# Performance work log

Measured on AMD Instinct MI355X. Metric: run time of the kernel, lower is better.

The kernel has to match this reference:

```python
import jax, jax.numpy as jnp
import numpy as np

# Model constants (from init_kwargs / _select_heads)
H = 8          # heads for dim=1024
KR = 16        # read/write top-k
CHUNK = 128    # chunk size for chunked memory update
ETA = 0.1      # update rate
FORGET = 0.01  # decay_lambda -> forget_base per chunk
LWIN = 512     # local_window = K (use_bypass=True)


def _l2norm(t, eps=1e-6):
    return t / (jnp.linalg.norm(t, axis=-1, keepdims=True) + eps)


def setup_inputs() -> dict:
    key = jax.random.key(0)
    ks = jax.random.split(key, 5)
    B, T, D, K = 2, 2048, 1024, 512
    x = jax.random.normal(ks[0], (B, T, D), dtype=jnp.float32)
    W_qkv = jax.random.normal(ks[1], (3 * D, D), dtype=jnp.float32) / np.sqrt(D)
    b_qkv = jnp.zeros((3 * D,), dtype=jnp.float32)
    W_o = jax.random.normal(ks[2], (D, D), dtype=jnp.float32) / np.sqrt(D)
    b_o = jnp.zeros((D,), dtype=jnp.float32)
    S_init = jax.random.normal(ks[3], (K, D), dtype=jnp.float32) / np.sqrt(D)
    read_temperature = jnp.ones((1,), dtype=jnp.float32)
    return {"x": x, "W_qkv": W_qkv, "b_qkv": b_qkv, "W_o": W_o,
            "b_o": b_o, "S_init": S_init, "read_temperature": read_temperature}


def reference(x, W_qkv, b_qkv, W_o, b_o, S_init, read_temperature):
    B, T, D = x.shape
    K = S_init.shape[0]
    dh = D // H
    scale = 1.0 / np.sqrt(dh)
    temp = read_temperature[0]

    # fused qkv projection, split to heads [B,H,T,dh]
    qkv = x @ W_qkv.T + b_qkv
    q, k, v = jnp.split(qkv, 3, axis=-1)
    to_h = lambda t: t.reshape(B, T, H, dh).transpose(0, 2, 1, 3)
    qh, kh, vh = to_h(q), to_h(k), to_h(v)

    # initial slot state from S_init: [K, D] -> [H, K, dh] -> [B,H,K,dh]
    slot = S_init.reshape(K, H, dh).transpose(1, 0, 2)
    slot_k0 = jnp.broadcast_to(_l2norm(slot), (B, H, K, dh))
    slot_v0 = jnp.broadcast_to(slot, (B, H, K, dh))

    nc = T // CHUNK
    # [nc, B, H, C, dh]
    to_c = lambda t: t.reshape(B, H, nc, CHUNK, dh).transpose(2, 0, 1, 3, 4)
    qc, kc, vc = to_c(qh), to_c(kh), to_c(vh)

    bi_g = jnp.arange(B)[:, None, None, None]   # gather indices
    hi_g = jnp.arange(H)[None, :, None, None]
    bi_s = jnp.arange(B)[:, None, None]         # scatter indices
    hi_s = jnp.arange(H)[None, :, None]

    def chunk_step(carry, inp):
        slot_k, slot_v = carry
        qt, kt, vt = inp  # [B,H,C,dh]
        # ---- top-k sparse read from slot memory ----
        rscores = jnp.einsum('bhcd,bhkd->bhck', qt, slot_k) * scale / temp
        rv, ri = jax.lax.top_k(rscores, KR)
        rp = jax.nn.softmax(rv, axis=-1)                 # [B,H,C,KR]
        sel_v = slot_v[bi_g, hi_g, ri]                   # [B,H,C,KR,dh]
        read = jnp.einsum('bhck,bhckd->bhcd', rp, sel_v)
        # ---- top-k write with orthogonal update + decay ----
        k_hat = _l2norm(kt)
        wscores = jnp.einsum('bhcd,bhkd->bhck', k_hat, slot_k)
        wv, wi = jax.lax.top_k(wscores, KR)
        wp = jax.nn.softmax(wv, axis=-1)
        sel_k = slot_k[bi_g, hi_g, wi]                   # [B,H,C,KR,dh]
        proj = jnp.einsum('bhcd,bhckd->bhck', vt, sel_k)
        v_orth = vt[:, :, :, None, :] - proj[..., None] * sel_k
        dv = ETA * wp[..., None] * v_orth                # [B,H,C,KR,dh]
        dk = ETA * wp[..., None] * (k_hat[:, :, :, None, :] - sel_k)
        idx = wi.reshape(B, H, CHUNK * KR)
        slot_v = (1.0 - FORGET) * slot_v
        slot_v = slot_v.at[bi_s, hi_s, idx].add(dv.reshape(B, H, CHUNK * KR, dh))
        slot_k = _l2norm(slot_k.at[bi_s, hi_s, idx].add(dk.reshape(B, H, CHUNK * KR, dh)))
        return (slot_k, slot_v), read

    _, reads = jax.lax.scan(chunk_step, (slot_k0, slot_v0), (qc, kc, vc))
    reads = reads.transpose(1, 2, 0, 3, 4).reshape(B, H, T, dh)

    # ---- local bypass: block-causal sliding-window attention (window=LWIN) ----
    nb = T // LWIN
    qb = qh.reshape(B, H, nb, LWIN, dh)
    kb = kh.reshape(B, H, nb, LWIN, dh)
    vb = vh.reshape(B, H, nb, LWIN, dh)
    zpad = jnp.zeros_like(kb[:, :, :1])
    kcat = jnp.concatenate([jnp.concatenate([zpad, kb[:, :, :-1]], axis=2), kb], axis=3)
    vcat = jnp.concatenate([jnp.concatenate([zpad, vb[:, :, :-1]], axis=2), vb], axis=3)
    s = jnp.einsum('bhnqd,bhnkd->bhnqk', qb, kcat) * scale  # [B,H,nb,LWIN,2*LWIN]
    i = jnp.arange(LWIN)[:, None]
    j = jnp.arange(2 * LWIN)[None, :]
    base = (j <= LWIN + i) & (j > i)                        # causal + window
    blk = (jnp.arange(nb) > 0)[:, None, None] | (j >= LWIN)[None]
    mask = base[None] & blk                                 # [nb,LWIN,2*LWIN]
    s = jnp.where(mask[None, None], s, -1e30)
    a = jax.nn.softmax(s, axis=-1)
    local = jnp.einsum('bhnqk,bhnkd->bhnqd', a, vcat).reshape(B, H, T, dh)

    y = (reads + local).transpose(0, 2, 1, 3).reshape(B, T, D)
    return y @ W_o.T + b_o
```

## Files before the change

### kernel.cpp

```cpp
#include <hip/hip_runtime.h>

typedef unsigned short u16;
typedef unsigned int u32;
typedef unsigned long long u64;
typedef __attribute__((ext_vector_type(8))) short bf16x8;
typedef __attribute__((ext_vector_type(4))) float f32x4;

#define B2 2
#define T2 2048
#define D2 1024
#define H2 8
#define DH 128
#define KSL 512
#define CH 128
#define NCH 16
#define NBH 16
#define MAGIC 0x13579BDFu

__device__ __forceinline__ float bf2f(u32 h) { union { u32 u; float f; } x; x.u = h << 16; return x.f; }
__device__ __forceinline__ u16 f2bf(float f) {
  union { float f; u32 u; } x; x.f = f;
  return (u16)((x.u + 0x7FFFu + ((x.u >> 16) & 1u)) >> 16);
}
__device__ __forceinline__ u32 pack2(float a, float b) { return (u32)f2bf(a) | ((u32)f2bf(b) << 16); }

__device__ __forceinline__ u32 cload32(const void* p) {
  return __hip_atomic_load((u32*)p, __ATOMIC_RELAXED, __HIP_MEMORY_SCOPE_AGENT);
}
__device__ __forceinline__ void cstore32(void* p, u32 v) {
  __hip_atomic_store((u32*)p, v, __ATOMIC_RELAXED, __HIP_MEMORY_SCOPE_AGENT);
}
__device__ __forceinline__ u64 cload64(const void* p) {
  return __hip_atomic_load((u64*)p, __ATOMIC_RELAXED, __HIP_MEMORY_SCOPE_AGENT);
}
__device__ __forceinline__ void cstore64(void* p, u64 v) {
  __hip_atomic_store((u64*)p, v, __ATOMIC_RELAXED, __HIP_MEMORY_SCOPE_AGENT);
}
__device__ __forceinline__ float2 cloadf2(const float* p) {
  union { u64 q; float2 f; } x; x.q = cload64(p); return x.f;
}
__device__ __forceinline__ void cstoref2(float* p, float2 v) {
  union { float2 f; u64 q; } x; x.f = v; cstore64(p, x.q);
}

__global__ __launch_bounds__(256) void qkv_gemm(
    const float* __restrict__ x, const float* __restrict__ w,
    const float* __restrict__ bias, u16* __restrict__ qhb,
    u16* __restrict__ khb, u16* __restrict__ vhb) {
  __shared__ u16 As[128 * 72];
  __shared__ u16 Bs[128 * 72];
  const int tid = threadIdx.x;
  const int lane = tid & 63, wv = tid >> 6;
  const int quad = lane >> 4, l15 = lane & 15;
  const int m0 = blockIdx.y * 128, n0 = blockIdx.x * 128;
  const int wr = wv >> 1, wc = wv & 1;
  f32x4 acc[4][4];
#pragma unroll
  for (int i = 0; i < 4; ++i)
#pragma unroll
    for (int j = 0; j < 4; ++j) acc[i][j] = f32x4{0.f, 0.f, 0.f, 0.f};
  const int f4c = tid & 15, r0 = tid >> 4;
  for (int kt = 0; kt < 16; ++kt) {
#pragma unroll
    for (int i = 0; i < 8; ++i) {
      int row = r0 + i * 16;
      float4 a = *(const float4*)(x + (size_t)(m0 + row) * 1024 + kt * 64 + f4c * 4);
      float4 b = *(const float4*)(w + (size_t)(n0 + row) * 1024 + kt * 64 + f4c * 4);
      *(uint2*)(&As[row * 72 + f4c * 4]) = make_uint2(pack2(a.x, a.y), pack2(a.z, a.w));
      *(uint2*)(&Bs[row * 72 + f4c * 4]) = make_uint2(pack2(b.x, b.y), pack2(b.z, b.w));
    }
    __syncthreads();
#pragma unroll
    for (int ks = 0; ks < 2; ++ks) {
      bf16x8 af[4], bff[4];
#pragma unroll
      for (int rt = 0; rt < 4; ++rt)
        af[rt] = *(const bf16x8*)(&As[(wr * 64 + rt * 16 + l15) * 72 + ks * 32 + quad * 8]);
#pragma unroll
      for (int ct = 0; ct < 4; ++ct)
        bff[ct] = *(const bf16x8*)(&Bs[(wc * 64 + ct * 16 + l15) * 72 + ks * 32 + quad * 8]);
#pragma unroll
      for (int rt = 0; rt < 4; ++rt)
#pragma unroll
        for (int ct = 0; ct < 4; ++ct)
          acc[rt][ct] = __builtin_amdgcn_mfma_f32_16x16x32_bf16(af[rt], bff[ct], acc[rt][ct], 0, 0, 0);
    }
    __syncthreads();
  }
#pragma unroll
  for (int ct = 0; ct < 4; ++ct) {
    int n = n0 + wc * 64 + ct * 16 + l15;
    float bv = bias[n];
    int sec = n >> 10, rr2 = n & 1023, hh = rr2 >> 7, dd = rr2 & 127;
    u16* dst = (sec == 0) ? qhb : (sec == 1) ? khb : vhb;
#pragma unroll
    for (int rt = 0; rt < 4; ++rt)
#pragma unroll
      for (int rg = 0; rg < 4; ++rg) {
        int m = m0 + wr * 64 + rt * 16 + quad * 4 + rg;
        int bb = m >> 11, tt = m & 2047;
        dst[((size_t)(bb * 8 + hh) * T2 + tt) * DH + dd] = f2bf(acc[rt][ct][rg] + bv);
      }
  }
}

__global__ __launch_bounds__(256) void attn_kernel(
    const u16* __restrict__ qhb, const u16* __restrict__ khb,
    const u16* __restrict__ vhb, float* __restrict__ yin) {
  __shared__ u16 Pls[128 * 72];
  __shared__ u16 VT[128 * 72];
  const int tid = threadIdx.x;
  const int lane = tid & 63, wv = tid >> 6;
  const int quad = lane >> 4, l15 = lane & 15;
  const int bh = blockIdx.y, qt = blockIdx.x;
  const int t0 = qt * 128;
  const int b = bh >> 3, h = bh & 7;
  f32x4 Oa[2][8];
  float mrow[2][4], lrow[2][4];
#pragma unroll
  for (int rt = 0; rt < 2; ++rt) {
#pragma unroll
    for (int dt = 0; dt < 8; ++dt) Oa[rt][dt] = f32x4{0.f, 0.f, 0.f, 0.f};
#pragma unroll
    for (int rg = 0; rg < 4; ++rg) { mrow[rt][rg] = -1e30f; lrow[rt][rg] = 0.f; }
  }
  const u16* qbase = qhb + ((size_t)bh * T2 + t0) * DH;
  int j0 = t0 / 64 - 8; if (j0 < 0) j0 = 0;
  int j1 = t0 / 64 + 1;
  for (int jt = j0; jt <= j1; ++jt) {
    int kv0 = jt * 64;
    __syncthreads();
    {
      int r = tid & 63, dq = tid >> 6;
      const u16* vrow = vhb + ((size_t)bh * T2 + kv0 + r) * DH + dq * 32;
#pragma unroll
      for (int u = 0; u < 4; ++u) {
        uint4 pv = *(const uint4*)(vrow + u * 8);
        int d0 = dq * 32 + u * 8;
        VT[(d0 + 0) * 72 + r] = (u16)(pv.x); VT[(d0 + 1) * 72 + r] = (u16)(pv.x >> 16);
        VT[(d0 + 2) * 72 + r] = (u16)(pv.y); VT[(d0 + 3) * 72 + r] = (u16)(pv.y >> 16);
        VT[(d0 + 4) * 72 + r] = (u16)(pv.z); VT[(d0 + 5) * 72 + r] = (u16)(pv.z >> 16);
        VT[(d0 + 6) * 72 + r] = (u16)(pv.w); VT[(d0 + 7) * 72 + r] = (u16)(pv.w >> 16);
      }
    }
    f32x4 Sa[2][4];
#pragma unroll
    for (int rt = 0; rt < 2; ++rt)
#pragma unroll
      for (int ct = 0; ct < 4; ++ct) Sa[rt][ct] = f32x4{0.f, 0.f, 0.f, 0.f};
#pragma unroll
    for (int ks = 0; ks < 4; ++ks) {
      bf16x8 a0 = *(const bf16x8*)(qbase + (size_t)(wv * 32 + l15) * DH + ks * 32 + quad * 8);
      bf16x8 a1 = *(const bf16x8*)(qbase + (size_t)(wv * 32 + 16 + l15) * DH + ks * 32 + quad * 8);
#pragma unroll
      for (int ct = 0; ct < 4; ++ct) {
        bf16x8 bb = *(const bf16x8*)(khb + ((size_t)bh * T2 + kv0 + ct * 16 + l15) * DH + ks * 32 + quad * 8);
        Sa[0][ct] = __builtin_amdgcn_mfma_f32_16x16x32_bf16(a0, bb, Sa[0][ct], 0, 0, 0);
        Sa[1][ct] = __builtin_amdgcn_mfma_f32_16x16x32_bf16(a1, bb, Sa[1][ct], 0, 0, 0);
      }
    }
#pragma unroll
    for (int rt = 0; rt < 2; ++rt)
#pragma unroll
      for (int rg = 0; rg < 4; ++rg) {
        int row = wv * 32 + rt * 16 + quad * 4 + rg;
        int qp = t0 + row;
        float vals[4];
        float mx = -1e30f;
#pragma unroll
        for (int ct = 0; ct < 4; ++ct) {
          int kp = kv0 + ct * 16 + l15;
          float s = Sa[rt][ct][rg] * 0.08838834764831845f;
          bool ok = (kp <= qp) && (kp + 512 > qp);
          s = ok ? s : -1e30f;
          vals[ct] = s;
          mx = fmaxf(mx, s);
        }
#pragma unroll
        for (int sh = 1; sh < 16; sh <<= 1) mx = fmaxf(mx, __shfl_xor(mx, sh));
        float mold = mrow[rt][rg];
        float mnew = fmaxf(mold, mx);
        float alpha = __expf(mold - mnew);
        float rsum = 0.f;
        float pv_[4];
#pragma unroll
        for (int ct = 0; ct < 4; ++ct) {
          float p = (vals[ct] < -1e29f) ? 0.f : __expf(vals[ct] - mnew);
          pv_[ct] = p; rsum += p;
        }
#pragma unroll
        for (int sh = 1; sh < 16; sh <<= 1) rsum += __shfl_xor(rsum, sh);
        lrow[rt][rg] = lrow[rt][rg] * alpha + rsum;
        mrow[rt][rg] = mnew;
#pragma unroll
        for (int dt = 0; dt < 8; ++dt) Oa[rt][dt][rg] *= alpha;
#pragma unroll
        for (int ct = 0; ct < 4; ++ct) Pls[row * 72 + ct * 16 + l15] = f2bf(pv_[ct]);
      }
    __syncthreads();
#pragma unroll
    for (int ks = 0; ks < 2; ++ks) {
      bf16x8 a0 = *(const bf16x8*)(&Pls[(wv * 32 + l15) * 72 + ks * 32 + quad * 8]);
      bf16x8 a1 = *(const bf16x8*)(&Pls[(wv * 32 + 16 + l15) * 72 + ks * 32 + quad * 8]);
#pragma unroll
      for (int dt = 0; dt < 8; ++dt) {
        bf16x8 bb = *(const bf16x8*)(&VT[(dt * 16 + l15) * 72 + ks * 32 + quad * 8]);
        Oa[0][dt] = __builtin_amdgcn_mfma_f32_16x16x32_bf16(a0, bb, Oa[0][dt], 0, 0, 0);
        Oa[1][dt] = __builtin_amdgcn_mfma_f32_16x16x32_bf16(a1, bb, Oa[1][dt], 0, 0, 0);
      }
    }
  }
#pragma unroll
  for (int rt = 0; rt < 2; ++rt)
#pragma unroll
    for (int rg = 0; rg < 4; ++rg) {
      int row = wv * 32 + rt * 16 + quad * 4 + rg;
      float invl = 1.0f / lrow[rt][rg];
#pragma unroll
      for (int dt = 0; dt < 8; ++dt)
        yin[((size_t)b * T2 + t0 + row) * D2 + h * DH + dt * 16 + l15] = Oa[rt][dt][rg] * invl;
    }
}

struct ScanArgs {
  const u16* qhb; const u16* khb; const u16* vhb;
  float* yin; float* sk; float* sv; u16* skb; u16* khatb;
  u32* cnt; uint4* entries;
  u32* barcnt; u32* bargen; u32* ready;
  const float* sinit; const float* temp;
};

__device__ __forceinline__ void bh_barrier(u32* cnt, u32* gen) {
  asm volatile("" ::: "memory");
  __syncthreads();
  if (threadIdx.x == 0) {
    u32 g = cload32(gen);
    u32 a = __hip_atomic_fetch_add(cnt, 1u, __ATOMIC_RELAXED, __HIP_MEMORY_SCOPE_AGENT);
    if ((a & 15u) == 15u) {
      cstore32(gen, g + 1u);
    } else {
      while (cload32(gen) == g) __builtin_amdgcn_s_sleep(2);
    }
    __builtin_amdgcn_fence(__ATOMIC_ACQUIRE, "agent");
  }
  __syncthreads();
  asm volatile("" ::: "memory");
}

__device__ __forceinline__ void topk16(const float* rowp, int lane, volatile u64* candw,
                                       float& p_out, u32& idx_out) {
  u32 mono[8];
#pragma unroll
  for (int j = 0; j < 8; ++j) {
    float f = rowp[j * 64 + lane];
    u32 u = __float_as_uint(f);
    mono[j] = ((int)u < 0) ? ~u : (u | 0x80000000u);
  }
  u32 mx = mono[0];
#pragma unroll
  for (int j = 1; j < 8; ++j) mx = max(mx, mono[j]);
  u32 s = mx;
#pragma unroll
  for (int k = 2; k <= 64; k <<= 1) {
#pragma unroll
    for (int j = k >> 1; j > 0; j >>= 1) {
      u32 o = (u32)__shfl_xor((int)s, j);
      bool keep_min = (((lane & k) == 0) == ((lane & j) == 0));
      u32 mn = min(s, o), mxx = max(s, o);
      s = keep_min ? mn : mxx;
    }
  }
  u32 thr = (u32)__shfl((int)s, 48);
  u32 base = 0;
#pragma unroll
  for (int j = 0; j < 8; ++j) {
    bool pred = (mono[j] >= thr);
    u64 mask = __ballot(pred);
    u32 pos = base + (u32)__popcll(mask & ((1ull << lane) - 1ull));
    if (pred && pos < 64u)
      candw[pos] = (((u64)mono[j]) << 32) | (u64)(0xFFFFFFFFu - (u32)(j * 64 + lane));
    base += (u32)__popcll(mask);
  }
  __threadfence_block();
  u32 cntc = base < 64u ? base : 64u;
  u64 key = ((u32)lane < cntc) ? candw[lane] : 0ull;
#pragma unroll
  for (int k = 2; k <= 64; k <<= 1) {
#pragma unroll
    for (int j = k >> 1; j > 0; j >>= 1) {
      u64 o = __shfl_xor(key, j);
      bool keep_min = (((lane & k) == 0) == ((lane & j) == 0));
      u64 mn = key < o ? key : o;
      u64 mxx = key < o ? o : key;
      key = keep_min ? mn : mxx;
    }
  }
  u32 um = (u32)(key >> 32);
  float val = __uint_as_float((um & 0x80000000u) ? (um & 0x7FFFFFFFu) : ~um);
  idx_out = 0xFFFFFFFFu - (u32)(key & 0xFFFFFFFFull);
  float mtop = __shfl(val, 63);
  float e = __expf(val - mtop);
  float ssum = e;
#pragma unroll
  for (int sh = 1; sh < 16; sh <<= 1) ssum += __shfl_xor(ssum, sh);
  p_out = e / ssum;
}

__global__ __launch_bounds__(512, 2) void scan_kernel(ScanArgs A) {
  const int tid = threadIdx.x;
  const int lane = tid & 63, wv = tid >> 6;
  const int quad = lane >> 4, l15 = lane & 15;
  const int xcd = blockIdx.x & 7;
  const int wi = blockIdx.x >> 3;
  const int bh = xcd * 2 + (wi >> 4);
  const int blk = wi & 15;
  const int b = bh >> 3, h = bh & 7;
  __shared__ u16 khat_ls[8 * 136];
  __shared__ float scores_r[8 * 520];
  __shared__ float scores_w[8 * 520];
  __shared__ u64 cand[8][64];

  const float invtemp = 1.0f / A.temp[0];
  const float sc_r = 0.08838834764831845f * invtemp;

#pragma unroll 1
  for (int i = 0; i < 4; ++i) {
    int s = blk * 32 + wv * 4 + i;
    float2 v2 = *(const float2*)(A.sinit + (size_t)s * 1024 + h * 128 + lane * 2);
    float ssq = v2.x * v2.x + v2.y * v2.y;
#pragma unroll
    for (int sh = 1; sh < 64; sh <<= 1) ssq += __shfl_xor(ssq, sh);
    float inv = 1.0f / (sqrtf(ssq) + 1e-6f);
    size_t off = ((size_t)bh * KSL + s) * DH + lane * 2;
    cstoref2(A.sk + off, make_float2(v2.x * inv, v2.y * inv));
    cstoref2(A.sv + off, v2);
    cstore32(A.skb + off, pack2(v2.x * inv, v2.y * inv));
    if (lane == 0) cstore32(&A.cnt[bh * KSL + s], 0u);
  }
  if (blk == 0 && tid == 0) { cstore32(A.barcnt + bh, 0u); cstore32(A.bargen + bh, 0u); }
  __syncthreads();
  if (tid == 0) {
    cstore32(&A.ready[bh * 16 + blk], MAGIC);
    for (int i = 0; i < 16; ++i)
      while (cload32(&A.ready[bh * 16 + i]) != MAGIC) __builtin_amdgcn_s_sleep(2);
    __builtin_amdgcn_fence(__ATOMIC_ACQUIRE, "agent");
  }
  __syncthreads();

  u32* bcnt = A.barcnt + bh;
  u32* bgen = A.bargen + bh;

#pragma unroll 1
  for (int ci = 0; ci < NCH; ++ci) {
    const int t0base = ci * CH;
    const int c = blk * 8 + wv;
    const int trow = t0base + c;
    {
      u32 kraw = *(const u32*)(A.khb + ((size_t)bh * T2 + trow) * DH + lane * 2);
      float k0 = bf2f(kraw & 0xFFFFu), k1 = bf2f(kraw >> 16);
      float ssq = k0 * k0 + k1 * k1;
#pragma unroll
      for (int sh = 1; sh < 64; sh <<= 1) ssq += __shfl_xor(ssq, sh);
      float inv = 1.0f / (sqrtf(ssq) + 1e-6f);
      u32 pk = pack2(k0 * inv, k1 * inv);
      *(u32*)(&khat_ls[wv * 136 + lane * 2]) = pk;
      cstore32(A.khatb + ((size_t)bh * CH + c) * DH + lane * 2, pk);
    }
    __syncthreads();
    {
      const u16* qbase = A.qhb + ((size_t)bh * T2 + t0base + blk * 8) * DH;
      const u16* sbase = A.skb + (size_t)bh * KSL * DH;
      f32x4 acc[4];
#pragma unroll
      for (int ct = 0; ct < 4; ++ct) acc[ct] = f32x4{0.f, 0.f, 0.f, 0.f};
#pragma unroll
      for (int ks = 0; ks < 4; ++ks) {
        bf16x8 a;
        if (l15 < 8)
          a = *(const bf16x8*)(qbase + (size_t)l15 * DH + ks * 32 + quad * 8);
        else
          a = *(const bf16x8*)(&khat_ls[(l15 - 8) * 136 + ks * 32 + quad * 8]);
#pragma unroll
        for (int ct = 0; ct < 4; ++ct) {
          bf16x8 bb = *(const bf16x8*)(sbase + (size_t)(wv * 64 + ct * 16 + l15) * DH + ks * 32 + quad * 8);
          acc[ct] = __builtin_amdgcn_mfma_f32_16x16x32_bf16(a, bb, acc[ct], 0, 0, 0);
        }
      }
#pragma unroll
      for (int ct = 0; ct < 4; ++ct)
#pragma unroll
        for (int rg = 0; rg < 4; ++rg) {
          int m = quad * 4 + rg;
          int col = wv * 64 + ct * 16 + l15;
          if (m < 8) scores_r[m * 520 + col] = acc[ct][rg] * sc_r;
          else       scores_w[(m - 8) * 520 + col] = acc[ct][rg];
        }
    }
    __syncthreads();
    {
      float p; u32 sidx;
      topk16(&scores_r[wv * 520], lane, cand[wv], p, sidx);
      float acc0 = 0.f, acc1 = 0.f;
      const float* svb = A.sv + (size_t)bh * KSL * DH;
#pragma unroll
      for (int r = 0; r < 16; ++r) {
        float pr = __shfl(p, 63 - r);
        u32 ir = (u32)__shfl((int)sidx, 63 - r);
        float2 vv = *(const float2*)(svb + (size_t)ir * DH + lane * 2);
        acc0 += pr * vv.x; acc1 += pr * vv.y;
      }
      {
        float* yp = A.yin + ((size_t)b * T2 + trow) * D2 + h * DH + lane * 2;
        float2 y0 = cloadf2(yp);
        cstoref2(yp, make_float2(y0.x + acc0, y0.y + acc1));
      }

      float wp; u32 widx;
      topk16(&scores_w[wv * 520], lane, cand[wv], wp, widx);
      const int r = lane >> 2, g = lane & 3;
      float wr = __shfl(wp, 63 - r);
      u32 ir = (u32)__shfl((int)widx, 63 - r);
      const float* kb = A.sk + ((size_t)bh * KSL + ir) * DH + g * 32;
      const u16* vb = A.vhb + ((size_t)bh * T2 + trow) * DH + g * 32;
      float part = 0.f;
#pragma unroll
      for (int u2 = 0; u2 < 4; ++u2) {
        uint4 vvp = *(const uint4*)(vb + u2 * 8);
        float4 k0 = *(const float4*)(kb + u2 * 8);
        float4 k1 = *(const float4*)(kb + u2 * 8 + 4);
        part += bf2f(vvp.x & 0xFFFFu) * k0.x + bf2f(vvp.x >> 16) * k0.y
              + bf2f(vvp.y & 0xFFFFu) * k0.z + bf2f(vvp.y >> 16) * k0.w
              + bf2f(vvp.z & 0xFFFFu) * k1.x + bf2f(vvp.z >> 16) * k1.y
              + bf2f(vvp.w & 0xFFFFu) * k1.z + bf2f(vvp.w >> 16) * k1.w;
      }
      part += __shfl_xor(part, 1);
      part += __shfl_xor(part, 2);
      if (g == 0) {
        u32 pos = __hip_atomic_fetch_add(&A.cnt[bh * KSL + ir], 1u,
                                         __ATOMIC_RELAXED, __HIP_MEMORY_SCOPE_AGENT);
        if (pos < 128u) {
          u32* e = (u32*)(A.entries + ((size_t)bh * KSL + ir) * 128 + pos);
          cstore64(e, (u64)(u32)c | ((u64)__float_as_uint(wr) << 32));
          cstore32(e + 2, __float_as_uint(part));
        }
      }
    }
    bh_barrier(bcnt, bgen);
    {
      u32 n4[4]; size_t soff4[4];
      uint4 eL0[4], eL1[4];
#pragma unroll
      for (int i = 0; i < 4; ++i) {
        soff4[i] = (size_t)bh * KSL + blk * 32 + wv * 4 + i;
        n4[i] = cload32(&A.cnt[soff4[i]]);
        const uint4* eb = A.entries + soff4[i] * 128;
        eL0[i] = eb[lane];
        eL1[i] = eb[64 + lane];
      }
#pragma unroll
      for (int i = 0; i < 4; ++i) {
        size_t roff = soff4[i] * DH + lane * 2;
        float2 V = *(const float2*)(A.sv + roff);
        float2 Kr = *(const float2*)(A.sk + roff);
        u32 nd = n4[i] < 128u ? n4[i] : 128u;
        float dv0 = 0, dv1 = 0, dk0 = 0, dk1 = 0;
#pragma unroll 1
        for (u32 b2 = 0; b2 < nd; b2 += 16) {
          u32 m = nd - b2; if (m > 16u) m = 16u;
          u32 sx = (b2 < 64u) ? eL0[i].x : eL1[i].x;
          u32 sy = (b2 < 64u) ? eL0[i].y : eL1[i].y;
          u32 sz = (b2 < 64u) ? eL0[i].z : eL1[i].z;
          u32 vr[16], hr[16];
#pragma unroll
          for (int j = 0; j < 16; ++j) if (j < (int)m) {
            u32 src = (b2 + (u32)j) & 63u;
            u32 c2 = (u32)__shfl((int)sx, (int)src);
            vr[j] = *(const u32*)(A.vhb + ((size_t)bh * T2 + t0base + c2) * DH + lane * 2);
            hr[j] = *(const u32*)(A.khatb + ((size_t)bh * CH + c2) * DH + lane * 2);
          }
#pragma unroll
          for (int j = 0; j < 16; ++j) if (j < (int)m) {
            u32 src = (b2 + (u32)j) & 63u;
            float wpe = __uint_as_float((u32)__shfl((int)sy, (int)src));
            float pj = __uint_as_float((u32)__shfl((int)sz, (int)src));
            dv0 += wpe * (bf2f(vr[j] & 0xFFFFu) - pj * Kr.x);
            dv1 += wpe * (bf2f(vr[j] >> 16) - pj * Kr.y);
            dk0 += wpe * (bf2f(hr[j] & 0xFFFFu) - Kr.x);
            dk1 += wpe * (bf2f(hr[j] >> 16) - Kr.y);
          }
        }
        cstoref2(A.sv + roff, make_float2(0.99f * V.x + 0.1f * dv0, 0.99f * V.y + 0.1f * dv1));
        if (n4[i] > 0u) {
          float u0 = Kr.x + 0.1f * dk0, u1 = Kr.y + 0.1f * dk1;
          float ssq = u0 * u0 + u1 * u1;
#pragma unroll
          for (int sh = 1; sh < 64; sh <<= 1) ssq += __shfl_xor(ssq, sh);
          float inv = 1.0f / (sqrtf(ssq) + 1e-6f);
          u0 *= inv; u1 *= inv;
          cstoref2(A.sk + roff, make_float2(u0, u1));
          cstore32(A.skb + roff, pack2(u0, u1));
        }
        if (lane == 0) cstore32(&A.cnt[soff4[i]], 0u);
      }
    }
    bh_barrier(bcnt, bgen);
  }
}

__global__ __launch_bounds__(256) void out_gemm(
    const float* __restrict__ yin, const float* __restrict__ w,
    const float* __restrict__ bias, float* __restrict__ out) {
  __shared__ u16 As[128 * 72];
  __shared__ u16 Bs[128 * 72];
  const int tid = threadIdx.x;
  const int lane = tid & 63, wv = tid >> 6;
  const int quad = lane >> 4, l15 = lane & 15;
  const int m0 = blockIdx.y * 128, n0 = blockIdx.x * 128;
  const int wr = wv >> 1, wc = wv & 1;
  f32x4 acc[4][4];
#pragma unroll
  for (int i = 0; i < 4; ++i)
#pragma unroll
    for (int j = 0; j < 4; ++j) acc[i][j] = f32x4{0.f, 0.f, 0.f, 0.f};
  const int f4c = tid & 15, r0 = tid >> 4;
  for (int kt = 0; kt < 16; ++kt) {
#pragma unroll
    for (int i = 0; i < 8; ++i) {
      int row = r0 + i * 16;
      float4 a = *(const float4*)(yin + (size_t)(m0 + row) * 1024 + kt * 64 + f4c * 4);
      float4 b = *(const float4*)(w + (size_t)(n0 + row) * 1024 + kt * 64 + f4c * 4);
      *(uint2*)(&As[row * 72 + f4c * 4]) = make_uint2(pack2(a.x, a.y), pack2(a.z, a.w));
      *(uint2*)(&Bs[row * 72 + f4c * 4]) = make_uint2(pack2(b.x, b.y), pack2(b.z, b.w));
    }
    __syncthreads();
#pragma unroll
    for (int ks = 0; ks < 2; ++ks) {
      bf16x8 af[4], bff[4];
#pragma unroll
      for (int rt = 0; rt < 4; ++rt)
        af[rt] = *(const bf16x8*)(&As[(wr * 64 + rt * 16 + l15) * 72 + ks * 32 + quad * 8]);
#pragma unroll
      for (int ct = 0; ct < 4; ++ct)
        bff[ct] = *(const bf16x8*)(&Bs[(wc * 64 + ct * 16 + l15) * 72 + ks * 32 + quad * 8]);
#pragma unroll
      for (int rt = 0; rt < 4; ++rt)
#pragma unroll
        for (int ct = 0; ct < 4; ++ct)
          acc[rt][ct] = __builtin_amdgcn_mfma_f32_16x16x32_bf16(af[rt], bff[ct], acc[rt][ct], 0, 0, 0);
    }
    __syncthreads();
  }
#pragma unroll
  for (int ct = 0; ct < 4; ++ct) {
    int n = n0 + wc * 64 + ct * 16 + l15;
    float bv = bias[n];
#pragma unroll
    for (int rt = 0; rt < 4; ++rt)
#pragma unroll
      for (int rg = 0; rg < 4; ++rg) {
        int m = m0 + wr * 64 + rt * 16 + quad * 4 + rg;
        out[(size_t)m * 1024 + n] = acc[rt][ct][rg] + bv;
      }
  }
}

extern "C" void kernel_launch(void* const* d_in, const int* in_sizes, int n_in,
                              void* d_out, int out_size, void* d_ws, size_t ws_size,
                              hipStream_t stream) {
  const float* x = (const float*)d_in[0];
  const float* Wqkv = (const float*)d_in[1];
  const float* bqkv = (const float*)d_in[2];
  const float* Wo = (const float*)d_in[3];
  const float* bo = (const float*)d_in[4];
  const float* Sinit = (const float*)d_in[5];
  const float* temp = (const float*)d_in[6];
  float* out = (float*)d_out;

  char* p = (char*)d_ws;
  auto take = [&](size_t bytes) { char* r = p; p += (bytes + 255) & ~(size_t)255; return r; };
  u16* qhb = (u16*)take((size_t)NBH * T2 * DH * 2);
  u16* khb = (u16*)take((size_t)NBH * T2 * DH * 2);
  u16* vhb = (u16*)take((size_t)NBH * T2 * DH * 2);
  float* yin = (float*)take((size_t)B2 * T2 * D2 * 4);
  float* sk = (float*)take((size_t)NBH * KSL * DH * 4);
  float* sv = (float*)take((size_t)NBH * KSL * DH * 4);
  u16* skb = (u16*)take((size_t)NBH * KSL * DH * 2);
  u16* khatb = (u16*)take((size_t)NBH * CH * DH * 2);
  u32* cnt = (u32*)take((size_t)NBH * KSL * 4);
  uint4* entries = (uint4*)take((size_t)NBH * KSL * 128 * 16);
  u32* barcnt = (u32*)take(64 * 4);
  u32* bargen = (u32*)take(64 * 4);
  u32* ready = (u32*)take(NBH * 16 * 4);

  hipLaunchKernelGGL(qkv_gemm, dim3(24, 32), dim3(256), 0, stream, x, Wqkv, bqkv, qhb, khb, vhb);
  hipLaunchKernelGGL(attn_kernel, dim3(16, 16), dim3(256), 0, stream, qhb, khb, vhb, yin);
  ScanArgs sa{qhb, khb, vhb, yin, sk, sv, skb, khatb, cnt, entries, barcnt, bargen, ready, Sinit, temp};
  hipLaunchKernelGGL(scan_kernel, dim3(256), dim3(512), 0, stream, sa);
  hipLaunchKernelGGL(out_gemm, dim3(8, 32), dim3(256), 0, stream, yin, Wo, bo, out);
}
```

Baseline: 706.7 us.

## Interleave dual top-k selection, widen slot-update batch, relax barrier acquire

Merges the read and write top-k selections into one interleaved routine so two independent shuffle sorting networks run side by side and hide each other's latency. The yin load is issued before the gather loop rather than after it. The slot-update gather batch grows from 16 to 32 entries to keep more loads in flight, and spin-wait sleeps are shortened. The acquire fence is dropped from the first per-chunk barrier and launch bounds change to one block per CU, which raises register headroom but may expose stale-cache reads if the coherence loads do not cover every access.

```diff
diff --git a/kernel.cpp b/kernel.cpp
--- a/kernel.cpp
+++ b/kernel.cpp
@@ -230,7 +230,7 @@
   const float* sinit; const float* temp;
 };
 
-__device__ __forceinline__ void bh_barrier(u32* cnt, u32* gen) {
+__device__ __forceinline__ void bh_barrier(u32* cnt, u32* gen, bool do_inv) {
   asm volatile("" ::: "memory");
   __syncthreads();
   if (threadIdx.x == 0) {
@@ -239,74 +239,105 @@
     if ((a & 15u) == 15u) {
       cstore32(gen, g + 1u);
     } else {
-      while (cload32(gen) == g) __builtin_amdgcn_s_sleep(2);
-    }
-    __builtin_amdgcn_fence(__ATOMIC_ACQUIRE, "agent");
+      while (cload32(gen) == g) __builtin_amdgcn_s_sleep(1);
+    }
+    if (do_inv)
+      __builtin_amdgcn_fence(__ATOMIC_ACQUIRE, "agent");
   }
   __syncthreads();
   asm volatile("" ::: "memory");
 }
 
-__device__ __forceinline__ void topk16(const float* rowp, int lane, volatile u64* candw,
-                                       float& p_out, u32& idx_out) {
-  u32 mono[8];
+__device__ __forceinline__ void topk16_dual(
+    const float* rp0, const float* rp1, int lane,
+    volatile u64* cw0, volatile u64* cw1,
+    float& p0_out, u32& i0_out, float& p1_out, u32& i1_out) {
+  u32 mono[2][8];
 #pragma unroll
   for (int j = 0; j < 8; ++j) {
-    float f = rowp[j * 64 + lane];
-    u32 u = __float_as_uint(f);
-    mono[j] = ((int)u < 0) ? ~u : (u | 0x80000000u);
-  }
-  u32 mx = mono[0];
-#pragma unroll
-  for (int j = 1; j < 8; ++j) mx = max(mx, mono[j]);
-  u32 s = mx;
+    u32 u0 = __float_as_uint(rp0[j * 64 + lane]);
+    u32 u1 = __float_as_uint(rp1[j * 64 + lane]);
+    mono[0][j] = ((int)u0 < 0) ? ~u0 : (u0 | 0x80000000u);
+    mono[1][j] = ((int)u1 < 0) ? ~u1 : (u1 | 0x80000000u);
+  }
+  u32 sv_[2];
+#pragma unroll
+  for (int s = 0; s < 2; ++s) {
+    u32 mx = mono[s][0];
+#pragma unroll
+    for (int j = 1; j < 8; ++j) mx = max(mx, mono[s][j]);
+    sv_[s] = mx;
+  }
 #pragma unroll
   for (int k = 2; k <= 64; k <<= 1) {
 #pragma unroll
     for (int j = k >> 1; j > 0; j >>= 1) {
-      u32 o = (u32)__shfl_xor((int)s, j);
-      bool keep_min = (((lane & k) == 0) == ((lane & j) == 0));
-      u32 mn = min(s, o), mxx = max(s, o);
-      s = keep_min ? mn : mxx;
-    }
-  }
-  u32 thr = (u32)__shfl((int)s, 48);
-  u32 base = 0;
+      bool km = (((lane & k) == 0) == ((lane & j) == 0));
+#pragma unroll
+      for (int s = 0; s < 2; ++s) {
+        u32 o = (u32)__shfl_xor((int)sv_[s], j);
+        u32 mn = min(sv_[s], o), mxx = max(sv_[s], o);
+        sv_[s] = km ? mn : mxx;
+      }
+    }
+  }
+  u32 thr[2] = { (u32)__shfl((int)sv_[0], 48), (u32)__shfl((int)sv_[1], 48) };
+  u32 base[2] = { 0u, 0u };
 #pragma unroll
   for (int j = 0; j < 8; ++j) {
-    bool pred = (mono[j] >= thr);
-    u64 mask = __ballot(pred);
-    u32 pos = base + (u32)__popcll(mask & ((1ull << lane) - 1ull));
-    if (pred && pos < 64u)
-      candw[pos] = (((u64)mono[j]) << 32) | (u64)(0xFFFFFFFFu - (u32)(j * 64 + lane));
-    base += (u32)__popcll(mask);
+#pragma unroll
+    for (int s = 0; s < 2; ++s) {
+      bool pred = (mono[s][j] >= thr[s]);
+      u64 mask = __ballot(pred);
+      u32 pos = base[s] + (u32)__popcll(mask & ((1ull << lane) - 1ull));
+      volatile u64* cw = s ? cw1 : cw0;
+      if (pred && pos < 64u)
+        cw[pos] = (((u64)mono[s][j]) << 32) | (u64)(0xFFFFFFFFu - (u32)(j * 64 + lane));
+      base[s] += (u32)__popcll(mask);
+    }
   }
   __threadfence_block();
-  u32 cntc = base < 64u ? base : 64u;
-  u64 key = ((u32)lane < cntc) ? candw[lane] : 0ull;
+  u64 key[2];
+  {
+    u32 c0 = base[0] < 64u ? base[0] : 64u;
+    u32 c1 = base[1] < 64u ? base[1] : 64u;
+    key[0] = ((u32)lane < c0) ? cw0[lane] : 0ull;
+    key[1] = ((u32)lane < c1) ? cw1[lane] : 0ull;
+  }
 #pragma unroll
   for (int k = 2; k <= 64; k <<= 1) {
 #pragma unroll
     for (int j = k >> 1; j > 0; j >>= 1) {
-      u64 o = __shfl_xor(key, j);
-      bool keep_min = (((lane & k) == 0) == ((lane & j) == 0));
-      u64 mn = key < o ? key : o;
-      u64 mxx = key < o ? o : key;
-      key = keep_min ? mn : mxx;
-    }
-  }
-  u32 um = (u32)(key >> 32);
-  float val = __uint_as_float((um & 0x80000000u) ? (um & 0x7FFFFFFFu) : ~um);
-  idx_out = 0xFFFFFFFFu - (u32)(key & 0xFFFFFFFFull);
-  float mtop = __shfl(val, 63);
-  float e = __expf(val - mtop);
-  float ssum = e;
-#pragma unroll
-  for (int sh = 1; sh < 16; sh <<= 1) ssum += __shfl_xor(ssum, sh);
-  p_out = e / ssum;
-}
-
-__global__ __launch_bounds__(512, 2) void scan_kernel(ScanArgs A) {
+      bool km = (((lane & k) == 0) == ((lane & j) == 0));
+#pragma unroll
+      for (int s = 0; s < 2; ++s) {
+        u64 o = __shfl_xor(key[s], j);
+        u64 mn = key[s] < o ? key[s] : o;
+        u64 mxx = key[s] < o ? o : key[s];
+        key[s] = km ? mn : mxx;
+      }
+    }
+  }
+  float e[2], ssum[2]; u32 idx[2];
+#pragma unroll
+  for (int s = 0; s < 2; ++s) {
+    u32 um = (u32)(key[s] >> 32);
+    float val = __uint_as_float((um & 0x80000000u) ? (um & 0x7FFFFFFFu) : ~um);
+    idx[s] = 0xFFFFFFFFu - (u32)(key[s] & 0xFFFFFFFFull);
+    float mtop = __shfl(val, 63);
+    e[s] = __expf(val - mtop);
+    ssum[s] = e[s];
+  }
+#pragma unroll
+  for (int sh = 1; sh < 16; sh <<= 1) {
+    ssum[0] += __shfl_xor(ssum[0], sh);
+    ssum[1] += __shfl_xor(ssum[1], sh);
+  }
+  p0_out = e[0] / ssum[0]; i0_out = idx[0];
+  p1_out = e[1] / ssum[1]; i1_out = idx[1];
+}
+
+__global__ __launch_bounds__(512, 1) void scan_kernel(ScanArgs A) {
   const int tid = threadIdx.x;
   const int lane = tid & 63, wv = tid >> 6;
   const int quad = lane >> 4, l15 = lane & 15;
@@ -318,7 +349,8 @@
   __shared__ u16 khat_ls[8 * 136];
   __shared__ float scores_r[8 * 520];
   __shared__ float scores_w[8 * 520];
-  __shared__ u64 cand[8][64];
+  __shared__ u64 cand0[8][64];
+  __shared__ u64 cand1[8][64];
 
   const float invtemp = 1.0f / A.temp[0];
   const float sc_r = 0.08838834764831845f * invtemp;
@@ -342,7 +374,7 @@
   if (tid == 0) {
     cstore32(&A.ready[bh * 16 + blk], MAGIC);
     for (int i = 0; i < 16; ++i)
-      while (cload32(&A.ready[bh * 16 + i]) != MAGIC) __builtin_amdgcn_s_sleep(2);
+      while (cload32(&A.ready[bh * 16 + i]) != MAGIC) __builtin_amdgcn_s_sleep(1);
     __builtin_amdgcn_fence(__ATOMIC_ACQUIRE, "agent");
   }
   __syncthreads();
@@ -398,8 +430,11 @@
     }
     __syncthreads();
     {
-      float p; u32 sidx;
-      topk16(&scores_r[wv * 520], lane, cand[wv], p, sidx);
+      float p, wp; u32 sidx, widx;
+      topk16_dual(&scores_r[wv * 520], &scores_w[wv * 520], lane,
+                  cand0[wv], cand1[wv], p, sidx, wp, widx);
+      float* yp = A.yin + ((size_t)b * T2 + trow) * D2 + h * DH + lane * 2;
+      float2 y0 = *(const float2*)yp;
       float acc0 = 0.f, acc1 = 0.f;
       const float* svb = A.sv + (size_t)bh * KSL * DH;
 #pragma unroll
@@ -409,14 +444,8 @@
         float2 vv = *(const float2*)(svb + (size_t)ir * DH + lane * 2);
         acc0 += pr * vv.x; acc1 += pr * vv.y;
       }
-      {
-        float* yp = A.yin + ((size_t)b * T2 + trow) * D2 + h * DH + lane * 2;
-        float2 y0 = cloadf2(yp);
-        cstoref2(yp, make_float2(y0.x + acc0, y0.y + acc1));
-      }
-
-      float wp; u32 widx;
-      topk16(&scores_w[wv * 520], lane, cand[wv], wp, widx);
+      cstoref2(yp, make_float2(y0.x + acc0, y0.y + acc1));
+
       const int r = lane >> 2, g = lane & 3;
       float wr = __shfl(wp, 63 - r);
       u32 ir = (u32)__shfl((int)widx, 63 - r);
@@ -445,7 +474,7 @@
         }
       }
     }
-    bh_barrier(bcnt, bgen);
+    bh_barrier(bcnt, bgen, false);
     {
       u32 n4[4]; size_t soff4[4];
       uint4 eL0[4], eL1[4];
@@ -465,21 +494,21 @@
         u32 nd = n4[i] < 128u ? n4[i] : 128u;
         float dv0 = 0, dv1 = 0, dk0 = 0, dk1 = 0;
 #pragma unroll 1
-        for (u32 b2 = 0; b2 < nd; b2 += 16) {
-          u32 m = nd - b2; if (m > 16u) m = 16u;
+        for (u32 b2 = 0; b2 < nd; b2 += 32) {
+          u32 m = nd - b2; if (m > 32u) m = 32u;
           u32 sx = (b2 < 64u) ? eL0[i].x : eL1[i].x;
           u32 sy = (b2 < 64u) ? eL0[i].y : eL1[i].y;
           u32 sz = (b2 < 64u) ? eL0[i].z : eL1[i].z;
-          u32 vr[16], hr[16];
-#pragma unroll
-          for (int j = 0; j < 16; ++j) if (j < (int)m) {
+          u32 vr[32], hr[32];
+#pragma unroll
+          for (int j = 0; j < 32; ++j) if (j < (int)m) {
             u32 src = (b2 + (u32)j) & 63u;
             u32 c2 = (u32)__shfl((int)sx, (int)src);
             vr[j] = *(const u32*)(A.vhb + ((size_t)bh * T2 + t0base + c2) * DH + lane * 2);
             hr[j] = *(const u32*)(A.khatb + ((size_t)bh * CH + c2) * DH + lane * 2);
           }
 #pragma unroll
-          for (int j = 0; j < 16; ++j) if (j < (int)m) {
+          for (int j = 0; j < 32; ++j) if (j < (int)m) {
             u32 src = (b2 + (u32)j) & 63u;
             float wpe = __uint_as_float((u32)__shfl((int)sy, (int)src));
             float pj = __uint_as_float((u32)__shfl((int)sz, (int)src));
@@ -503,7 +532,7 @@
         if (lane == 0) cstore32(&A.cnt[soff4[i]], 0u);
       }
     }
-    bh_barrier(bcnt, bgen);
+    bh_barrier(bcnt, bgen, true);
   }
 }
 
```

After: 779.8 us. 1.1x slower.
